# Kernel optimization log

Measured on AMD Instinct MI355X. Metric: run time of the kernel, lower is better.

## Reference

```python
import jax, jax.numpy as jnp
import numpy as np

N = 50000      # nodes
E = 800000     # edges
H = 8          # heads
D = 16         # per-head dim (hidden_channels)
HD = H * D     # 128
G = 64         # graphs in batch
BN_EPS = 1e-5


def setup_inputs() -> dict:
    key = jax.random.key(0)
    ks = iter(jax.random.split(key, 40))
    s = lambda *shape: jax.random.normal(next(ks), shape, dtype=jnp.float32) * 0.05
    inp = {
        "X": jax.random.normal(next(ks), (N, 1), dtype=jnp.float32),
        "edge_index": jax.random.randint(next(ks), (2, E), 0, N, dtype=jnp.int32),
        "batch": jnp.sort(jax.random.randint(next(ks), (N,), 0, G, dtype=jnp.int32)),
        # layer 1: in=1 -> H*D
        "Wq1": s(1, HD), "bq1": jnp.zeros((HD,), jnp.float32),
        "Wk1": s(1, HD), "bk1": jnp.zeros((HD,), jnp.float32),
        "Wv1": s(1, HD), "bv1": jnp.zeros((HD,), jnp.float32),
        "Ws1": s(1, HD), "bs1": jnp.zeros((HD,), jnp.float32),
        # layers 2-5 stacked: in=HD -> H*D
        "Wq": s(4, HD, HD), "bq": jnp.zeros((4, HD), jnp.float32),
        "Wk": s(4, HD, HD), "bk": jnp.zeros((4, HD), jnp.float32),
        "Wv": s(4, HD, HD), "bv": jnp.zeros((4, HD), jnp.float32),
        "Ws": s(4, HD, HD), "bs": jnp.zeros((4, HD), jnp.float32),
        # batchnorms (5 of them)
        "bn_gamma": jnp.ones((5, HD), jnp.float32),
        "bn_beta": jnp.zeros((5, HD), jnp.float32),
        "Wr": s(HD, 1), "br": jnp.zeros((1,), jnp.float32),
    }
    return inp


def _transformer_conv(x, src, dst, Wq, bq, Wk, bk, Wv, bv, Ws, bs):
    """PyG TransformerConv (concat=True, root_weight=True, beta=False), eval mode."""
    n = x.shape[0]
    q = (x @ Wq + bq).reshape(n, H, D)
    k = (x @ Wk + bk).reshape(n, H, D)
    v = (x @ Wv + bv).reshape(n, H, D)
    # per-edge attention logits: query at destination, key at source
    alpha = jnp.sum(q[dst] * k[src], axis=-1) / jnp.sqrt(jnp.float32(D))  # [E,H]
    # segment softmax over incoming edges of each destination node
    amax = jax.ops.segment_max(alpha, dst, num_segments=n)                # [N,H]
    amax = jnp.where(jnp.isfinite(amax), amax, 0.0)
    ex = jnp.exp(alpha - amax[dst])
    denom = jax.ops.segment_sum(ex, dst, num_segments=n) + 1e-16         # [N,H]
    w = ex / denom[dst]                                                  # [E,H]
    out = jax.ops.segment_sum(v[src] * w[:, :, None], dst, num_segments=n)  # [N,H,D]
    return out.reshape(n, HD) + (x @ Ws + bs)                            # root skip


def _bn(x, gamma, beta):
    mu = jnp.mean(x, axis=0)
    var = jnp.mean(jnp.square(x - mu), axis=0)  # biased, as torch BN training
    return (x - mu) * jax.lax.rsqrt(var + BN_EPS) * gamma + beta


def reference(X, edge_index, batch, Wq1, bq1, Wk1, bk1, Wv1, bv1, Ws1, bs1,
              Wq, bq, Wk, bk, Wv, bv, Ws, bs, bn_gamma, bn_beta, Wr, br):
    src, dst = edge_index[0], edge_index[1]
    x = jax.nn.relu(_transformer_conv(X, src, dst, Wq1, bq1, Wk1, bk1, Wv1, bv1, Ws1, bs1))
    x = _bn(x, bn_gamma[0], bn_beta[0])
    for i in range(4):  # layers 2..5 with residuals (dropout = identity in eval)
        h = jax.nn.relu(_transformer_conv(x, src, dst, Wq[i], bq[i], Wk[i], bk[i],
                                          Wv[i], bv[i], Ws[i], bs[i]))
        x = _bn(h, bn_gamma[i + 1], bn_beta[i + 1]) + x
    # global mean pool over graphs
    sums = jax.ops.segment_sum(x, batch, num_segments=G, indices_are_sorted=True)
    cnts = jax.ops.segment_sum(jnp.ones((x.shape[0],), x.dtype), batch,
                               num_segments=G, indices_are_sorted=True)
    x_mean = sums / jnp.maximum(cnts, 1.0)[:, None]
    pred = x_mean @ Wr + br
    return pred, x_mean
```

## Files before the change

kernel.cpp:

```cpp
#include <hip/hip_runtime.h>
#include <hip/hip_fp16.h>
#include <math.h>

#define HD 128
#define NGRAPH 64

typedef _Float16 f16x8 __attribute__((ext_vector_type(8)));
typedef _Float16 f16x2 __attribute__((ext_vector_type(2)));
typedef float    f32x4 __attribute__((ext_vector_type(4)));

__device__ __forceinline__ unsigned h2bits(__half2 h){ return *(unsigned*)&h; }

__device__ __forceinline__ float fdot2u(unsigned a, unsigned b, float c){
#if __has_builtin(__builtin_amdgcn_fdot2)
  return __builtin_amdgcn_fdot2(*(f16x2*)&a, *(f16x2*)&b, c, false);
#else
  float2 fa = __half22float2(*(__half2*)&a);
  float2 fb = __half22float2(*(__half2*)&b);
  return c + fa.x*fb.x + fa.y*fb.y;
#endif
}

__global__ __launch_bounds__(256) void k_count_setup(
    const int* __restrict__ dst, int* __restrict__ deg, int* __restrict__ epos, int E, int EB,
    const float* __restrict__ X,
    const float* __restrict__ Wq1, const float* __restrict__ bq1,
    const float* __restrict__ Wk1, const float* __restrict__ bk1,
    const float* __restrict__ Wv1, const float* __restrict__ bv1,
    const float* __restrict__ Ws1, const float* __restrict__ bs1,
    const float* __restrict__ Wq, const float* __restrict__ Wk,
    const float* __restrict__ Wv, const float* __restrict__ Ws,
    const int* __restrict__ batch, int* __restrict__ gstart,
    uint4* __restrict__ Wpack,
    unsigned* __restrict__ qh_u, unsigned* __restrict__ kvh_u, unsigned* __restrict__ h_u,
    int N, int L1B){
  int b = blockIdx.x;
  int tid = threadIdx.x;
  if (b < EB){
    int e = b*256 + tid;
    if (e < E) epos[e] = atomicAdd(&deg[dst[e]], 1);
  } else if (b < EB + L1B){
    int idx = (b - EB)*256 + tid;
    if (idx >= N*32) return;
    int n = idx >> 5, s4 = idx & 31, c = s4 << 2;
    float xv = X[n];
    float qv[4], kk[4], vv[4], hv[4];
    #pragma unroll
    for (int i = 0; i < 4; ++i){
      qv[i] = xv*Wq1[c+i] + bq1[c+i];
      kk[i] = xv*Wk1[c+i] + bk1[c+i];
      vv[i] = xv*Wv1[c+i] + bv1[c+i];
      hv[i] = xv*Ws1[c+i] + bs1[c+i];
    }
    uint2 hw;
    hw.x = h2bits(__floats2half2_rn(hv[0], hv[1]));
    hw.y = h2bits(__floats2half2_rn(hv[2], hv[3]));
    *(uint2*)&h_u[(size_t)n*64 + (c >> 1)] = hw;
    uint2 qw;
    qw.x = h2bits(__floats2half2_rn(qv[0], qv[1]));
    qw.y = h2bits(__floats2half2_rn(qv[2], qv[3]));
    *(uint2*)&qh_u[(size_t)n*64 + (c >> 1)] = qw;
    int head = c >> 4, ch = c & 15;
    size_t kbase = (size_t)n*128 + head*16 + (ch >> 1);
    uint2 kw, vw;
    kw.x = h2bits(__floats2half2_rn(kk[0], kk[1]));
    kw.y = h2bits(__floats2half2_rn(kk[2], kk[3]));
    vw.x = h2bits(__floats2half2_rn(vv[0], vv[1]));
    vw.y = h2bits(__floats2half2_rn(vv[2], vv[3]));
    *(uint2*)&kvh_u[kbase]     = kw;
    *(uint2*)&kvh_u[kbase + 8] = vw;
  } else if (b < EB + L1B + 128){
    int idx = (b - EB - L1B)*256 + tid;
    int mi   = idx >> 11;
    int rem  = idx & 2047;
    int lane = rem & 63;
    int tile = rem >> 6;
    int chunk = tile >> 3, nt = tile & 7;
    int l = mi >> 2, ws = mi & 3;
    const float* W = (ws==0?Wq:ws==1?Wk:ws==2?Wv:Ws) + (size_t)l*HD*HD;
    int quad = lane >> 4;
    int n = nt*16 + (lane & 15);
    int k0 = chunk*32 + quad*8;
    __half hs[8];
    #pragma unroll
    for (int j = 0; j < 8; ++j) hs[j] = __float2half(W[(size_t)(k0+j)*HD + n]);
    Wpack[idx] = *(uint4*)hs;
  } else {
    int g = tid;
    if (g > NGRAPH) return;
    int lo = 0, hi = N;
    while (lo < hi){
      int mid = (lo + hi) >> 1;
      if (batch[mid] < g) lo = mid + 1; else hi = mid;
    }
    gstart[g] = lo;
  }
}

__global__ __launch_bounds__(256) void k_scan1(const int* __restrict__ deg, int* __restrict__ rp,
                                               int* __restrict__ bt, int N){
  __shared__ int sm[256];
  int i = blockIdx.x*256 + threadIdx.x;
  int v = (i < N) ? deg[i] : 0;
  sm[threadIdx.x] = v;
  __syncthreads();
  for (int off = 1; off < 256; off <<= 1){
    int t = (threadIdx.x >= (unsigned)off) ? sm[threadIdx.x - off] : 0;
    __syncthreads();
    sm[threadIdx.x] += t;
    __syncthreads();
  }
  if (i < N) rp[i+1] = sm[threadIdx.x];
  if (threadIdx.x == 255) bt[blockIdx.x] = sm[255];
  if (blockIdx.x == 0 && threadIdx.x == 0) rp[0] = 0;
}

__global__ __launch_bounds__(256) void k_scan3(int* __restrict__ rp, const int* __restrict__ bt, int N){
  __shared__ int sm[256];
  int b = blockIdx.x, t = threadIdx.x;
  sm[t] = (t < b) ? bt[t] : 0;
  __syncthreads();
  for (int off = 128; off > 0; off >>= 1){
    if (t < off) sm[t] += sm[t + off];
    __syncthreads();
  }
  int offset = sm[0];
  int i = b*256 + t;
  if (i < N) rp[i+1] += offset;
}

__global__ __launch_bounds__(256) void k_scatter(const int* __restrict__ src, const int* __restrict__ dst,
                                                 const int* __restrict__ rp, const int* __restrict__ epos,
                                                 int* __restrict__ srcs, int E){
  int e = blockIdx.x*256 + threadIdx.x;
  if (e < E) srcs[rp[dst[e]] + epos[e]] = src[e];
}

__global__ __launch_bounds__(256) void k_stats(
    float* __restrict__ pr2, int layer, float* __restrict__ sclbb,
    const float* __restrict__ gamma, const float* __restrict__ beta, float invN){
  __shared__ float spos[256];
  int t = threadIdx.x;
  float* pb = pr2 + (size_t)(layer & 1)*16384;
  float s = 0.f;
  #pragma unroll 8
  for (int r = 0; r < 64; ++r) s += pb[r*256 + t];
  spos[t] = s;
  #pragma unroll 8
  for (int r = 0; r < 64; ++r) pb[r*256 + t] = 0.f;
  __syncthreads();
  if (t < 128){
    int c = t;
    int p = ((c & 15) << 3) | (c >> 4);
    float mu  = spos[p] * invN;
    float var = spos[128 + p] * invN - mu*mu;
    float scl = rsqrtf(var + 1e-5f) * gamma[c];
    sclbb[(layer & 1)*256 + c]       = scl;
    sclbb[(layer & 1)*256 + 128 + c] = beta[c] - mu*scl;
  }
}

__global__ __launch_bounds__(256) void k_gemm(
    const unsigned* __restrict__ hb_in, const unsigned* __restrict__ xold_u,
    unsigned* __restrict__ xnew_u,
    const uint4* __restrict__ Wpack, const float* __restrict__ sclbb,
    const float* __restrict__ bq, const float* __restrict__ bk,
    const float* __restrict__ bv, const float* __restrict__ bs,
    unsigned* __restrict__ qh_u, unsigned* __restrict__ kvh_u, unsigned* __restrict__ hskip_u,
    int N, int layer, int resid){
  __shared__ uint4 Bs[2048];
  int wsel = blockIdx.y;
  const uint4* Wm = Wpack + (size_t)(layer*4 + wsel)*2048;
  int tid = threadIdx.x;
  for (int i = tid; i < 2048; i += 256) Bs[i] = Wm[i];

  int w = tid >> 6, lane = tid & 63;
  int l15 = lane & 15, quad = lane >> 4;
  const float* bias = (wsel==0)?bq:(wsel==1)?bk:(wsel==2)?bv:bs;

  __syncthreads();

  for (int rt = 0; rt < 4; ++rt){
    int row0 = blockIdx.x*256 + w*64 + rt*16;
    if (row0 >= N) break;
    int arow = row0 + l15;

    f32x4 acc[8];
    #pragma unroll
    for (int i = 0; i < 8; ++i) acc[i] = (f32x4){0.f,0.f,0.f,0.f};

    #pragma unroll
    for (int chunk = 0; chunk < 4; ++chunk){
      uint4 au = {0u,0u,0u,0u};
      if (arow < N){
        int pbase = chunk*16 + quad*4;
        int cb = chunk*32 + quad*8;
        float4 s0 = *(const float4*)&sclbb[cb];
        float4 s1 = *(const float4*)&sclbb[cb + 4];
        float4 c0 = *(const float4*)&sclbb[128 + cb];
        float4 c1 = *(const float4*)&sclbb[128 + cb + 4];
        float scl[8] = {s0.x,s0.y,s0.z,s0.w, s1.x,s1.y,s1.z,s1.w};
        float bbv[8] = {c0.x,c0.y,c0.z,c0.w, c1.x,c1.y,c1.z,c1.w};
        uint4 hv = *(const uint4*)&hb_in[(size_t)arow*64 + pbase];
        unsigned hr[4] = {hv.x, hv.y, hv.z, hv.w};
        unsigned ap[4];
        if (resid){
          uint4 xv = *(const uint4*)&xold_u[(size_t)arow*64 + pbase];
          unsigned xr[4] = {xv.x, xv.y, xv.z, xv.w};
          #pragma unroll
          for (int j = 0; j < 4; ++j){
            float2 hf = __half22float2(*(__half2*)&hr[j]);
            float2 xf = __half22float2(*(__half2*)&xr[j]);
            float o0 = hf.x*scl[2*j]   + bbv[2*j]   + xf.x;
            float o1 = hf.y*scl[2*j+1] + bbv[2*j+1] + xf.y;
            ap[j] = h2bits(__floats2half2_rn(o0, o1));
          }
        } else {
          #pragma unroll
          for (int j = 0; j < 4; ++j){
            float2 hf = __half22float2(*(__half2*)&hr[j]);
            float o0 = hf.x*scl[2*j]   + bbv[2*j];
            float o1 = hf.y*scl[2*j+1] + bbv[2*j+1];
            ap[j] = h2bits(__floats2half2_rn(o0, o1));
          }
        }
        au.x = ap[0]; au.y = ap[1]; au.z = ap[2]; au.w = ap[3];
        if (wsel == 0) *(uint4*)&xnew_u[(size_t)arow*64 + pbase] = au;
      }
      f16x8 a = *(f16x8*)&au;
      #pragma unroll
      for (int nt = 0; nt < 8; ++nt){
        f16x8 bfr = *(const f16x8*)&Bs[(chunk*8 + nt)*64 + lane];
        acc[nt] = __builtin_amdgcn_mfma_f32_16x16x32_f16(a, bfr, acc[nt], 0, 0, 0);
      }
    }

    #pragma unroll
    for (int nt = 0; nt < 8; ++nt){
      int col = nt*16 + l15;
      float b = bias[col];
      #pragma unroll
      for (int reg = 0; reg < 4; ++reg){
        float val = acc[nt][reg] + b;
        float oth = __shfl_xor(val, 1);
        int row = row0 + quad*4 + reg;
        if (!(l15 & 1) && row < N){
          unsigned pk = h2bits(__floats2half2_rn(val, oth));
          if (wsel == 0)       qh_u[(size_t)row*64  + nt*8  + (l15>>1)]      = pk;
          else if (wsel == 1)  kvh_u[(size_t)row*128 + nt*16 + (l15>>1)]     = pk;
          else if (wsel == 2)  kvh_u[(size_t)row*128 + nt*16 + (l15>>1) + 8] = pk;
          else                 hskip_u[(size_t)row*64 + nt*8 + (l15>>1)]     = pk;
        }
      }
    }
  }
}

__global__ __launch_bounds__(256) void k_attn(
    const uint4* __restrict__ qh4, const uint4* __restrict__ kvh4,
    unsigned* __restrict__ h_u, float* __restrict__ pr2,
    const int* __restrict__ rp, const int* __restrict__ srcs, int N, int layer){
  __shared__ float ssum[4][128];
  __shared__ float ssq[4][128];
  int tid = threadIdx.x;
  int w = tid >> 6, lane = tid & 63;
  int oct = lane >> 3, hh = lane & 7;
  int n = blockIdx.x*4 + w;
  bool active = (n < N);

  float acc[16];
  #pragma unroll
  for (int i = 0; i < 16; ++i) acc[i] = 0.f;
  float lsum = 0.f;

  if (active){
    uint4 q0 = qh4[(size_t)n*16 + hh*2];
    uint4 q1 = qh4[(size_t)n*16 + hh*2 + 1];
    unsigned qr[8] = {q0.x,q0.y,q0.z,q0.w, q1.x,q1.y,q1.z,q1.w};
    int beg = rp[n], end = rp[n+1];
    int t = beg + oct;
    bool vcur = (t < end);
    uint4 g0, g1, g2, g3;
    if (vcur){
      const uint4* base = kvh4 + (size_t)srcs[t]*32 + hh*4;
      g0 = base[0]; g1 = base[1]; g2 = base[2]; g3 = base[3];
    }
    while (vcur){
      int tn = t + 8;
      bool vn = (tn < end);
      int sn = vn ? srcs[tn] : 0;
      const uint4* nb = kvh4 + (size_t)sn*32 + hh*4;
      uint4 n0 = nb[0], n1 = nb[1], n2 = nb[2], n3 = nb[3];

      unsigned kr[8] = {g0.x,g0.y,g0.z,g0.w, g1.x,g1.y,g1.z,g1.w};
      float pd = 0.f;
      #pragma unroll
      for (int i = 0; i < 8; ++i) pd = fdot2u(kr[i], qr[i], pd);
      float e = __expf(pd * 0.25f);
      lsum += e;
      unsigned vr[8] = {g2.x,g2.y,g2.z,g2.w, g3.x,g3.y,g3.z,g3.w};
      #pragma unroll
      for (int i = 0; i < 8; ++i){
        float2 vf = __half22float2(*(__half2*)&vr[i]);
        acc[2*i]   += e*vf.x;
        acc[2*i+1] += e*vf.y;
      }
      g0 = n0; g1 = n1; g2 = n2; g3 = n3;
      t = tn; vcur = vn;
    }
  }

  #pragma unroll
  for (int mask = 8; mask <= 32; mask <<= 1){
    lsum += __shfl_xor(lsum, mask);
    #pragma unroll
    for (int i = 0; i < 16; ++i) acc[i] += __shfl_xor(acc[i], mask);
  }
  float inv = (lsum > 0.f) ? 1.f/lsum : 0.f;

  float out[16];
  #pragma unroll
  for (int i = 0; i < 16; ++i) out[i] = 0.f;
  if (active && oct == 0){
    uint4* hp = (uint4*)(h_u + (size_t)n*64 + hh*8);
    uint4 s0 = hp[0], s1 = hp[1];
    unsigned sr[8] = {s0.x,s0.y,s0.z,s0.w, s1.x,s1.y,s1.z,s1.w};
    #pragma unroll
    for (int i = 0; i < 8; ++i){
      float2 sk = __half22float2(*(__half2*)&sr[i]);
      out[2*i]   = fmaxf(acc[2*i]*inv   + sk.x, 0.f);
      out[2*i+1] = fmaxf(acc[2*i+1]*inv + sk.y, 0.f);
    }
    uint4 w0, w1;
    w0.x = h2bits(__floats2half2_rn(out[0], out[1]));
    w0.y = h2bits(__floats2half2_rn(out[2], out[3]));
    w0.z = h2bits(__floats2half2_rn(out[4], out[5]));
    w0.w = h2bits(__floats2half2_rn(out[6], out[7]));
    w1.x = h2bits(__floats2half2_rn(out[8], out[9]));
    w1.y = h2bits(__floats2half2_rn(out[10], out[11]));
    w1.z = h2bits(__floats2half2_rn(out[12], out[13]));
    w1.w = h2bits(__floats2half2_rn(out[14], out[15]));
    hp[0] = w0; hp[1] = w1;
  }
  if (oct == 0){
    #pragma unroll
    for (int j = 0; j < 16; ++j){
      int pidx = j*8 + hh;
      ssum[w][pidx] = out[j];
      ssq[w][pidx]  = out[j]*out[j];
    }
  }
  __syncthreads();
  float* prow = pr2 + (size_t)(layer & 1)*16384 + (size_t)(blockIdx.x & 63)*256;
  if (tid < 128){
    atomicAdd(&prow[tid], ssum[0][tid]+ssum[1][tid]+ssum[2][tid]+ssum[3][tid]);
  } else {
    int c = tid - 128;
    atomicAdd(&prow[tid], ssq[0][c]+ssq[1][c]+ssq[2][c]+ssq[3][c]);
  }
}

__global__ __launch_bounds__(256) void k_pool1(
    const uint4* __restrict__ hb4, const uint4* __restrict__ xold4,
    const int* __restrict__ gstart, float* __restrict__ pp,
    const float* __restrict__ sclbb){
  __shared__ float sm[2048];
  __shared__ float sscl[128], sbb[128];
  int t = threadIdx.x;
  if (t < 128){
    sscl[t] = sclbb[t];
    sbb[t]  = sclbb[128 + t];
  }
  __syncthreads();
  int g = blockIdx.x, chunk = blockIdx.y;
  int tcol = t & 15, trow = t >> 4;
  int start = gstart[g];
  int endr  = gstart[g+1];
  int cb = tcol*8;
  float facc[8];
  #pragma unroll
  for (int j = 0; j < 8; ++j) facc[j] = 0.f;
  for (int r = start + chunk*16 + trow; r < endr; r += 64){
    uint4 hv = hb4[(size_t)r*16 + tcol];
    uint4 xv = xold4[(size_t)r*16 + tcol];
    unsigned hr[4] = {hv.x, hv.y, hv.z, hv.w};
    unsigned xr[4] = {xv.x, xv.y, xv.z, xv.w};
    #pragma unroll
    for (int j = 0; j < 4; ++j){
      float2 hf = __half22float2(*(__half2*)&hr[j]);
      float2 xf = __half22float2(*(__half2*)&xr[j]);
      facc[2*j]   += hf.x*sscl[cb+2*j]   + sbb[cb+2*j]   + xf.x;
      facc[2*j+1] += hf.y*sscl[cb+2*j+1] + sbb[cb+2*j+1] + xf.y;
    }
  }
  #pragma unroll
  for (int j = 0; j < 8; ++j) sm[t*8 + j] = facc[j];
  __syncthreads();
  if (t < 128){
    float s = 0.f;
    #pragma unroll
    for (int r = 0; r < 16; ++r) s += sm[r*128 + t];
    pp[(size_t)(g*4 + chunk)*128 + t] = s;
  }
}

__global__ __launch_bounds__(128) void k_pool2(
    const float* __restrict__ pp, const int* __restrict__ gstart,
    const float* __restrict__ Wr, const float* __restrict__ br,
    float* __restrict__ out){
  __shared__ float sm[128];
  int g = blockIdx.x, c = threadIdx.x;
  float s = 0.f;
  #pragma unroll
  for (int j = 0; j < 4; ++j) s += pp[(size_t)(g*4 + j)*128 + c];
  int cnt = gstart[g+1] - gstart[g];
  float xm = s / fmaxf((float)cnt, 1.f);
  out[NGRAPH + g*HD + c] = xm;
  sm[c] = xm * Wr[c];
  __syncthreads();
  for (int off = 64; off > 0; off >>= 1){
    if (c < off) sm[c] += sm[c + off];
    __syncthreads();
  }
  if (c == 0) out[g] = sm[0] + br[0];
}

extern "C" void kernel_launch(void* const* d_in, const int* in_sizes, int n_in,
                              void* d_out, int out_size, void* d_ws, size_t ws_size,
                              hipStream_t stream){
  const float* X     = (const float*)d_in[0];
  const int*   ei    = (const int*)  d_in[1];
  const int*   batch = (const int*)  d_in[2];
  const float* Wq1 = (const float*)d_in[3];  const float* bq1 = (const float*)d_in[4];
  const float* Wk1 = (const float*)d_in[5];  const float* bk1 = (const float*)d_in[6];
  const float* Wv1 = (const float*)d_in[7];  const float* bv1 = (const float*)d_in[8];
  const float* Ws1 = (const float*)d_in[9];  const float* bs1 = (const float*)d_in[10];
  const float* Wq  = (const float*)d_in[11]; const float* bq  = (const float*)d_in[12];
  const float* Wk  = (const float*)d_in[13]; const float* bk  = (const float*)d_in[14];
  const float* Wv  = (const float*)d_in[15]; const float* bv  = (const float*)d_in[16];
  const float* Ws  = (const float*)d_in[17]; const float* bs  = (const float*)d_in[18];
  const float* bn_g= (const float*)d_in[19]; const float* bn_b= (const float*)d_in[20];
  const float* Wr  = (const float*)d_in[21]; const float* br  = (const float*)d_in[22];

  const int N = in_sizes[0];
  const int E = in_sizes[1] / 2;

  const int* src = ei;
  const int* dst = ei + E;

  char* p = (char*)d_ws;
  auto alloc = [&](size_t bytes) -> void* {
    void* r = (void*)p;
    p += (bytes + 255) & ~(size_t)255;
    return r;
  };
  int*   deg  = (int*)alloc((size_t)N * 4);
  float* pr2  = (float*)alloc(2 * 64 * 256 * 4);
  char* zero_end = p;
  float* sclbb= (float*)alloc(2 * 256 * 4);
  int* rp     = (int*)alloc((size_t)(N + 1) * 4);
  int* bt     = (int*)alloc(256 * 4);
  int* gstart = (int*)alloc((NGRAPH + 1) * 4);
  int* epos   = (int*)alloc((size_t)E * 4);
  int* srcs   = (int*)alloc((size_t)E * 4);
  float* pp   = (float*)alloc((size_t)NGRAPH * 4 * 128 * 4);
  uint4* Wpack= (uint4*)alloc((size_t)16 * 2048 * 16);
  unsigned* qh_u  = (unsigned*)alloc((size_t)N * 64 * 4);
  unsigned* kvh_u = (unsigned*)alloc((size_t)N * 128 * 4);
  unsigned* hb0   = (unsigned*)alloc((size_t)N * 64 * 4);
  unsigned* hb1   = (unsigned*)alloc((size_t)N * 64 * 4);
  unsigned* xb0   = (unsigned*)alloc((size_t)N * 64 * 4);
  unsigned* xb1   = (unsigned*)alloc((size_t)N * 64 * 4);

  hipMemsetAsync(deg, 0, (size_t)(zero_end - (char*)deg), stream);

  const int NB  = (N + 255) / 256;
  const int EB  = (E + 255) / 256;
  const int L1B = (N * 32 + 255) / 256;
  const int NBLK = (N + 3) / 4;
  const float invN = 1.f / (float)N;

  unsigned* hb[2] = {hb0, hb1};
  unsigned* xb[2] = {xb0, xb1};

  k_count_setup<<<EB + L1B + 129, 256, 0, stream>>>(
      dst, deg, epos, E, EB,
      X, Wq1,bq1, Wk1,bk1, Wv1,bv1, Ws1,bs1,
      Wq, Wk, Wv, Ws, batch, gstart, Wpack, qh_u, kvh_u, hb0, N, L1B);
  k_scan1  <<<NB, 256, 0, stream>>>(deg, rp, bt, N);
  k_scan3  <<<NB, 256, 0, stream>>>(rp, bt, N);
  k_scatter<<<EB, 256, 0, stream>>>(src, dst, rp, epos, srcs, E);

  k_attn <<<NBLK, 256, 0, stream>>>((const uint4*)qh_u, (const uint4*)kvh_u, hb0, pr2, rp, srcs, N, 0);
  k_stats<<<1, 256, 0, stream>>>(pr2, 0, sclbb, bn_g, bn_b, invN);

  for (int l = 0; l < 4; ++l){
    k_gemm<<<dim3((N + 255) / 256, 4), 256, 0, stream>>>(
        hb[l & 1], xb[l & 1], xb[(l + 1) & 1],
        Wpack, sclbb + (size_t)(l & 1)*256,
        bq + (size_t)l*HD, bk + (size_t)l*HD, bv + (size_t)l*HD, bs + (size_t)l*HD,
        qh_u, kvh_u, hb[(l + 1) & 1],
        N, l, (l > 0) ? 1 : 0);
    k_attn <<<NBLK, 256, 0, stream>>>((const uint4*)qh_u, (const uint4*)kvh_u, hb[(l + 1) & 1],
                                      pr2, rp, srcs, N, l + 1);
    k_stats<<<1, 256, 0, stream>>>(pr2, l + 1, sclbb,
                                   bn_g + (size_t)(l+1)*HD, bn_b + (size_t)(l+1)*HD, invN);
  }

  k_pool1<<<dim3(NGRAPH, 4), 256, 0, stream>>>(
      (const uint4*)hb0, (const uint4*)xb0, gstart, pp, sclbb);
  k_pool2<<<NGRAPH, 128, 0, stream>>>(pp, gstart, Wr, br, (float*)d_out);
}
```

Before: 672.9 us.

## Compute BN-residual A tile once per block and loop over all four weight matrices

The GEMM kernel previously launched one grid slice per weight matrix (Q, K, V, skip), so each slice reloaded hb/xold and redid the batchnorm+residual prologue. Now each block handles 64 rows, builds the fp16 A fragments once in registers, and loops over the four weight matrices, reloading each into LDS behind barriers. This cuts A-side global reads and prologue math by four. In exchange each block does serial weight loads with extra syncs, and the grid has fewer, smaller-row blocks.

```diff
diff --git a/kernel.cpp b/kernel.cpp
--- a/kernel.cpp
+++ b/kernel.cpp
@@ -169,21 +169,66 @@
     unsigned* __restrict__ qh_u, unsigned* __restrict__ kvh_u, unsigned* __restrict__ hskip_u,
     int N, int layer, int resid){
   __shared__ uint4 Bs[2048];
-  int wsel = blockIdx.y;
-  const uint4* Wm = Wpack + (size_t)(layer*4 + wsel)*2048;
   int tid = threadIdx.x;
-  for (int i = tid; i < 2048; i += 256) Bs[i] = Wm[i];
-
   int w = tid >> 6, lane = tid & 63;
   int l15 = lane & 15, quad = lane >> 4;
-  const float* bias = (wsel==0)?bq:(wsel==1)?bk:(wsel==2)?bv:bs;
-
-  __syncthreads();
-
-  for (int rt = 0; rt < 4; ++rt){
-    int row0 = blockIdx.x*256 + w*64 + rt*16;
-    if (row0 >= N) break;
-    int arow = row0 + l15;
+  int row0 = blockIdx.x*64 + w*16;
+  int arow = row0 + l15;
+
+  const uint4* Wl = Wpack + (size_t)layer*4*2048;
+
+  for (int i = tid; i < 2048; i += 256) Bs[i] = Wl[i];
+
+  uint4 Areg[4];
+  #pragma unroll
+  for (int chunk = 0; chunk < 4; ++chunk){
+    uint4 au = {0u,0u,0u,0u};
+    if (arow < N){
+      int pbase = chunk*16 + quad*4;
+      int cb = chunk*32 + quad*8;
+      float4 s0 = *(const float4*)&sclbb[cb];
+      float4 s1 = *(const float4*)&sclbb[cb + 4];
+      float4 c0 = *(const float4*)&sclbb[128 + cb];
+      float4 c1 = *(const float4*)&sclbb[128 + cb + 4];
+      float scl[8] = {s0.x,s0.y,s0.z,s0.w, s1.x,s1.y,s1.z,s1.w};
+      float bbv[8] = {c0.x,c0.y,c0.z,c0.w, c1.x,c1.y,c1.z,c1.w};
+      uint4 hv = *(const uint4*)&hb_in[(size_t)arow*64 + pbase];
+      unsigned hr[4] = {hv.x, hv.y, hv.z, hv.w};
+      unsigned ap[4];
+      if (resid){
+        uint4 xv = *(const uint4*)&xold_u[(size_t)arow*64 + pbase];
+        unsigned xr[4] = {xv.x, xv.y, xv.z, xv.w};
+        #pragma unroll
+        for (int j = 0; j < 4; ++j){
+          float2 hf = __half22float2(*(__half2*)&hr[j]);
+          float2 xf = __half22float2(*(__half2*)&xr[j]);
+          float o0 = hf.x*scl[2*j]   + bbv[2*j]   + xf.x;
+          float o1 = hf.y*scl[2*j+1] + bbv[2*j+1] + xf.y;
+          ap[j] = h2bits(__floats2half2_rn(o0, o1));
+        }
+      } else {
+        #pragma unroll
+        for (int j = 0; j < 4; ++j){
+          float2 hf = __half22float2(*(__half2*)&hr[j]);
+          float o0 = hf.x*scl[2*j]   + bbv[2*j];
+          float o1 = hf.y*scl[2*j+1] + bbv[2*j+1];
+          ap[j] = h2bits(__floats2half2_rn(o0, o1));
+        }
+      }
+      au.x = ap[0]; au.y = ap[1]; au.z = ap[2]; au.w = ap[3];
+      *(uint4*)&xnew_u[(size_t)arow*64 + pbase] = au;
+    }
+    Areg[chunk] = au;
+  }
+
+  #pragma unroll
+  for (int ws = 0; ws < 4; ++ws){
+    if (ws > 0){
+      __syncthreads();
+      const uint4* Wm = Wl + (size_t)ws*2048;
+      for (int i = tid; i < 2048; i += 256) Bs[i] = Wm[i];
+    }
+    __syncthreads();
 
     f32x4 acc[8];
     #pragma unroll
@@ -191,43 +236,7 @@
 
     #pragma unroll
     for (int chunk = 0; chunk < 4; ++chunk){
-      uint4 au = {0u,0u,0u,0u};
-      if (arow < N){
-        int pbase = chunk*16 + quad*4;
-        int cb = chunk*32 + quad*8;
-        float4 s0 = *(const float4*)&sclbb[cb];
-        float4 s1 = *(const float4*)&sclbb[cb + 4];
-        float4 c0 = *(const float4*)&sclbb[128 + cb];
-        float4 c1 = *(const float4*)&sclbb[128 + cb + 4];
-        float scl[8] = {s0.x,s0.y,s0.z,s0.w, s1.x,s1.y,s1.z,s1.w};
-        float bbv[8] = {c0.x,c0.y,c0.z,c0.w, c1.x,c1.y,c1.z,c1.w};
-        uint4 hv = *(const uint4*)&hb_in[(size_t)arow*64 + pbase];
-        unsigned hr[4] = {hv.x, hv.y, hv.z, hv.w};
-        unsigned ap[4];
-        if (resid){
-          uint4 xv = *(const uint4*)&xold_u[(size_t)arow*64 + pbase];
-          unsigned xr[4] = {xv.x, xv.y, xv.z, xv.w};
-          #pragma unroll
-          for (int j = 0; j < 4; ++j){
-            float2 hf = __half22float2(*(__half2*)&hr[j]);
-            float2 xf = __half22float2(*(__half2*)&xr[j]);
-            float o0 = hf.x*scl[2*j]   + bbv[2*j]   + xf.x;
-            float o1 = hf.y*scl[2*j+1] + bbv[2*j+1] + xf.y;
-            ap[j] = h2bits(__floats2half2_rn(o0, o1));
-          }
-        } else {
-          #pragma unroll
-          for (int j = 0; j < 4; ++j){
-            float2 hf = __half22float2(*(__half2*)&hr[j]);
-            float o0 = hf.x*scl[2*j]   + bbv[2*j];
-            float o1 = hf.y*scl[2*j+1] + bbv[2*j+1];
-            ap[j] = h2bits(__floats2half2_rn(o0, o1));
-          }
-        }
-        au.x = ap[0]; au.y = ap[1]; au.z = ap[2]; au.w = ap[3];
-        if (wsel == 0) *(uint4*)&xnew_u[(size_t)arow*64 + pbase] = au;
-      }
-      f16x8 a = *(f16x8*)&au;
+      f16x8 a = *(f16x8*)&Areg[chunk];
       #pragma unroll
       for (int nt = 0; nt < 8; ++nt){
         f16x8 bfr = *(const f16x8*)&Bs[(chunk*8 + nt)*64 + lane];
@@ -235,6 +244,7 @@
       }
     }
 
+    const float* bias = (ws==0)?bq:(ws==1)?bk:(ws==2)?bv:bs;
     #pragma unroll
     for (int nt = 0; nt < 8; ++nt){
       int col = nt*16 + l15;
@@ -246,10 +256,10 @@
         int row = row0 + quad*4 + reg;
         if (!(l15 & 1) && row < N){
           unsigned pk = h2bits(__floats2half2_rn(val, oth));
-          if (wsel == 0)       qh_u[(size_t)row*64  + nt*8  + (l15>>1)]      = pk;
-          else if (wsel == 1)  kvh_u[(size_t)row*128 + nt*16 + (l15>>1)]     = pk;
-          else if (wsel == 2)  kvh_u[(size_t)row*128 + nt*16 + (l15>>1) + 8] = pk;
-          else                 hskip_u[(size_t)row*64 + nt*8 + (l15>>1)]     = pk;
+          if (ws == 0)       qh_u[(size_t)row*64  + nt*8  + (l15>>1)]      = pk;
+          else if (ws == 1)  kvh_u[(size_t)row*128 + nt*16 + (l15>>1)]     = pk;
+          else if (ws == 2)  kvh_u[(size_t)row*128 + nt*16 + (l15>>1) + 8] = pk;
+          else               hskip_u[(size_t)row*64 + nt*8 + (l15>>1)]     = pk;
         }
       }
     }
@@ -495,7 +505,7 @@
   k_stats<<<1, 256, 0, stream>>>(pr2, 0, sclbb, bn_g, bn_b, invN);
 
   for (int l = 0; l < 4; ++l){
-    k_gemm<<<dim3((N + 255) / 256, 4), 256, 0, stream>>>(
+    k_gemm<<<(N + 63) / 64, 256, 0, stream>>>(
         hb[l & 1], xb[l & 1], xb[(l + 1) & 1],
         Wpack, sclbb + (size_t)(l & 1)*256,
         bq + (size_t)l*HD, bk + (size_t)l*HD, bv + (size_t)l*HD, bs + (size_t)l*HD,
```

New measurement: 616.1 us (median of 2 runs). 8.4% less time.
